# Kernel optimization log

Measured on AMD Instinct MI355X. Metric: run time of the kernel, lower is better.

Reference implementation:

```python
import jax, jax.numpy as jnp
import numpy as np

N_ENT = 50000
N_REL = 500
N_EDGE = 640000
D_IN = 128
D_OUT = 128
NEG_SLOPE = 0.01  # torch nn.LeakyReLU default
BN_EPS = 1e-5


def setup_inputs() -> dict:
    key = jax.random.key(0)
    ks = jax.random.split(key, 16)
    edge_index = jax.random.randint(ks[0], (2, N_EDGE), 0, N_ENT)
    edge_type = jax.random.randint(ks[1], (N_EDGE,), 0, N_REL)
    query_type = jax.random.randint(ks[2], (N_EDGE,), 0, N_REL)
    entity_embed = jax.random.normal(ks[3], (N_ENT, D_IN), jnp.float32)
    rel_embed = jax.random.normal(ks[4], (N_REL, D_IN), jnp.float32)
    s = 0.05
    return {
        "edge_index": edge_index,
        "edge_type": edge_type,
        "query_type": query_type,
        "entity_embed": entity_embed,
        "rel_embed": rel_embed,
        "w_loop": jax.random.normal(ks[5], (D_IN, D_OUT), jnp.float32) * s,
        "w_out": jax.random.normal(ks[6], (D_IN, D_OUT), jnp.float32) * s,
        "w_rel": jax.random.normal(ks[7], (D_IN, D_OUT), jnp.float32) * s,
        "loop_rel": jax.random.normal(ks[8], (1, D_IN), jnp.float32) * s,
        "W_w": jax.random.normal(ks[9], (D_IN, D_IN), jnp.float32) * s,   # W.weight^T layout: x @ W_w
        "W_b": jnp.zeros((D_IN,), jnp.float32),
        "a_w": jax.random.normal(ks[10], (2 * D_IN, 1), jnp.float32) * s,
        "a_b": jnp.zeros((1,), jnp.float32),
        "bias": jnp.zeros((D_OUT,), jnp.float32),
        "bn_gamma": jnp.ones((D_OUT,), jnp.float32),
        "bn_beta": jnp.zeros((D_OUT,), jnp.float32),
    }


def _compgcn_fwd(edge_index, edge_type, query_type, entity_embed, rel_embed,
                 w_loop, w_out, w_rel, loop_rel, W_w, W_b, a_w, a_b,
                 bias, bn_gamma, bn_beta):
    N = entity_embed.shape[0]
    rel_all = jnp.concatenate([rel_embed, loop_rel], axis=0)  # (R+1, D)
    row, col = edge_index[0], edge_index[1]  # values already in [0, N)

    # edge norm: 1/out-degree of source node (deg[row] >= 1 for every edge)
    deg = jax.ops.segment_sum(jnp.ones((row.shape[0],), entity_embed.dtype), row, num_segments=N)
    norm = 1.0 / deg[row]  # (E,)

    # self-loop branch (mode='loop'): rel_transform 'mult' with loop relation, no attention
    loop_res = (entity_embed * rel_all[-1]) @ w_loop  # (N, D_out)

    # out branch (mode='out')
    x_j = entity_embed[col]          # (E, D)
    r_e = rel_all[edge_type]         # (E, D)
    q_e = rel_all[query_type]        # (E, D)
    xj_rel = x_j * r_e               # 'mult' composition

    h = jnp.concatenate([r_e @ W_w + W_b, q_e @ W_w + W_b], axis=-1)  # (E, 2D)
    logits = h @ a_w + a_b                                            # (E, 1)
    alpha = jnp.exp(jax.nn.leaky_relu(logits[:, 0], NEG_SLOPE))       # (E,)
    sum_alpha = jax.ops.segment_sum(alpha, row, num_segments=N)       # (N,)
    alpha = alpha / sum_alpha[row]

    msg = (xj_rel @ w_out) * (alpha * norm)[:, None]                  # (E, D_out)
    out_res = jax.ops.segment_sum(msg, row, num_segments=N)           # (N, D_out)

    out = 0.5 * out_res + 0.5 * loop_res + bias  # dropout = identity (eval)
    # BatchNorm1d, training-mode batch statistics (biased var), over node dim
    mean = jnp.mean(out, axis=0)
    var = jnp.mean((out - mean) ** 2, axis=0)
    out = (out - mean) * jax.lax.rsqrt(var + BN_EPS) * bn_gamma + bn_beta

    ent_out = jax.nn.leaky_relu(out, NEG_SLOPE)
    rel_out = (rel_all @ w_rel)[:-1]
    return ent_out, rel_out


def reference(edge_index, edge_type, query_type, entity_embed, rel_embed,
              w_loop, w_out, w_rel, loop_rel, W_w, W_b, a_w, a_b,
              bias, bn_gamma, bn_beta):
    return _compgcn_fwd(edge_index, edge_type, query_type, entity_embed, rel_embed,
                        w_loop, w_out, w_rel, loop_rel, W_w, W_b, a_w, a_b,
                        bias, bn_gamma, bn_beta)
```

## Files before the change

kernel.cpp:

```cpp
#include <hip/hip_runtime.h>
#include <math.h>

#define E_N 640000
#define N_N 50000
#define R_N 500
#define D   128
#define NEG 0.01f
#define BNEPS 1e-5f
#define CAP 48
#define GROUPS 8
#define RPG 6250

typedef _Float16 f16x8 __attribute__((ext_vector_type(8)));
typedef _Float16 h2 __attribute__((ext_vector_type(2)));
typedef float f32x4 __attribute__((ext_vector_type(4)));

#define CNT_OFF    0u
#define STAT_OFF   50000u
#define ZERO_FLOATS 50256u
#define BUCKET_OFF 50256u
#define ENTH_OFF   4850256u
#define RELH_OFF   8050256u
#define BT_OFF     8082256u
#define S1_OFF     8098640u
#define S2_OFF     8099152u
#define LOOPH_OFF  8099664u

__device__ __forceinline__ float lrelu(float x) { return x > 0.f ? x : NEG * x; }

__device__ __forceinline__ void st_f16x4(_Float16* p, float x, float y, float z, float w) {
    union { _Float16 h[4]; uint2 u; } pk;
    pk.h[0] = (_Float16)x; pk.h[1] = (_Float16)y; pk.h[2] = (_Float16)z; pk.h[3] = (_Float16)w;
    *(uint2*)p = pk.u;
}

__device__ __forceinline__ void st_f16x8(_Float16* p, const float* v) {
    union { _Float16 h[8]; uint4 u; } pk;
#pragma unroll
    for (int j = 0; j < 8; ++j) pk.h[j] = (_Float16)v[j];
    *(uint4*)p = pk.u;
}

#define P1_S   501
#define P1_WB  256
#define P1_REL 500
#define P1_ENT 1563

__global__ __launch_bounds__(128) void k_pre1(const float* __restrict__ Ww,
                                              const float* __restrict__ Wb,
                                              const float* __restrict__ aw,
                                              const float* __restrict__ rel,
                                              const float* __restrict__ looprel,
                                              const float* __restrict__ wout,
                                              const float* __restrict__ wloop,
                                              const float* __restrict__ wrel,
                                              const float* __restrict__ ent,
                                              float* __restrict__ s1,
                                              float* __restrict__ s2,
                                              _Float16* __restrict__ Bt,
                                              float* __restrict__ out_rel,
                                              _Float16* __restrict__ rel_h,
                                              _Float16* __restrict__ ent_h,
                                              _Float16* __restrict__ looprel_h) {
    int b = blockIdx.x, t = threadIdx.x;
    if (b < P1_S) {
        __shared__ float rr[D];
        __shared__ float part[4];
        const float* rp = (b < R_N) ? rel + (size_t)b * D : looprel;
        rr[t] = rp[t];
        if (b < R_N) rel_h[(size_t)b * D + t] = (_Float16)rp[t];
        if (b == R_N) looprel_h[t] = (_Float16)rp[t];
        __syncthreads();
        float v = 0.f;
        for (int i = 0; i < D; ++i) v = fmaf(rr[i], Ww[i * D + t], v);
        float p1 = aw[t] * v + Wb[t] * aw[t];
        float p2 = aw[D + t] * v + Wb[t] * aw[D + t];
        for (int o = 32; o; o >>= 1) {
            p1 += __shfl_down(p1, o);
            p2 += __shfl_down(p2, o);
        }
        if ((t & 63) == 0) {
            part[(t >> 6) * 2] = p1;
            part[(t >> 6) * 2 + 1] = p2;
        }
        __syncthreads();
        if (t == 0) {
            s1[b] = part[0] + part[2];
            s2[b] = part[1] + part[3];
        }
    } else if (b < P1_S + P1_WB) {
        int idx = (b - P1_S) * 128 + t;
        int n = idx & 127, k = idx >> 7;
        float v = (k < D) ? wout[(size_t)k * D + n] : wloop[(size_t)(k - D) * D + n];
        Bt[(size_t)n * 256 + k] = (_Float16)v;
    } else if (b < P1_S + P1_WB + P1_REL) {
        int r = b - (P1_S + P1_WB);
        __shared__ float rr2[D];
        rr2[t] = rel[(size_t)r * D + t];
        __syncthreads();
        float a = 0.f;
        for (int k = 0; k < D; ++k) a = fmaf(rr2[k], wrel[(size_t)k * D + t], a);
        out_rel[(size_t)r * D + t] = a;
    } else {
        int blk = b - (P1_S + P1_WB + P1_REL);
        const float4* e4 = (const float4*)ent;
#pragma unroll
        for (int j = 0; j < 8; ++j) {
            int idx = blk * 1024 + j * 128 + t;
            if (idx < N_N * D / 4) {
                float4 v = e4[idx];
                st_f16x4(ent_h + (size_t)idx * 4, v.x, v.y, v.z, v.w);
            }
        }
    }
}

#define BIN_NCH 313
#define BIN_BLOCKS (BIN_NCH * GROUPS)

__global__ __launch_bounds__(256) void k_bin(const int* __restrict__ row,
                                             const int* __restrict__ col,
                                             const int* __restrict__ et,
                                             const int* __restrict__ qt,
                                             const float* __restrict__ s1,
                                             const float* __restrict__ s2,
                                             const float* __restrict__ ab,
                                             int* __restrict__ cnt,
                                             int2* __restrict__ bucket) {
    int b = blockIdx.x, t = threadIdx.x;
    int g = b & 7;
    int chunk = b >> 3;
    int rlo = g * RPG;
    int e0 = chunk * 2048 + t;
    int r[8];
#pragma unroll
    for (int j = 0; j < 8; ++j) {
        int e = e0 + j * 256;
        r[j] = (e < E_N) ? row[e] : 0x7fffffff;
    }
#pragma unroll
    for (int j = 0; j < 8; ++j) {
        unsigned rr = (unsigned)(r[j] - rlo);
        if (rr < RPG) {
            int e = e0 + j * 256;
            int c = col[e], te = et[e], q = qt[e];
            float a = __expf(lrelu(s1[te] + s2[q] + ab[0]));
            int pos = atomicAdd(&cnt[r[j]], 1);
            if (pos < CAP) {
                bucket[(size_t)r[j] * CAP + pos] =
                    make_int2(c | (te << 16), __float_as_int(a));
            }
        }
    }
}

__global__ __launch_bounds__(128) void k_gather(const int* __restrict__ cnt,
                                                const int2* __restrict__ bucket,
                                                const _Float16* __restrict__ ent_h,
                                                const _Float16* __restrict__ rel_h,
                                                const _Float16* __restrict__ looprel_h,
                                                _Float16* __restrict__ stage) {
    int n = (blockIdx.x & 7) * RPG + (blockIdx.x >> 3);
    int t = threadIdx.x;
    int deg = cnt[n];
    int m = deg < CAP ? deg : CAP;
    __shared__ int eoff[CAP];
    __shared__ int roff[CAP];
    __shared__ h2 sah[CAP];
    __shared__ uint4 xred[16];
    float myv = 0.f;
    if (t < CAP) {
        if (t < m) {
            int2 be = bucket[(size_t)n * CAP + t];
            eoff[t] = (be.x & 0xffff) << 8;
            roff[t] = (be.x >> 16) << 8;
            float a = __int_as_float(be.y);
            myv = a;
            _Float16 ah = (_Float16)a;
            sah[t] = (h2){ah, ah};
        } else {
            eoff[t] = 0; roff[t] = 0;
            sah[t] = (h2){(_Float16)0.f, (_Float16)0.f};
        }
    }
    float suma = myv;
#pragma unroll
    for (int o = 1; o <= 32; o <<= 1) suma += __shfl_xor(suma, o);
    __syncthreads();
    int s = t & 15, g = t >> 4;
    const char* eb = (const char*)ent_h;
    const char* rb = (const char*)rel_h;
    int co = s * 16;
    h2 acc0 = (h2)(_Float16)0.f, acc1 = acc0, acc2 = acc0, acc3 = acc0;
#define EDGE(e_) { \
        uint4 ue = *(const uint4*)(eb + (eoff[e_] + co)); \
        uint4 ur = *(const uint4*)(rb + (roff[e_] + co)); \
        h2 a2 = sah[e_]; \
        const h2* e2 = (const h2*)&ue; \
        const h2* r2 = (const h2*)&ur; \
        acc0 += e2[0] * r2[0] * a2; \
        acc1 += e2[1] * r2[1] * a2; \
        acc2 += e2[2] * r2[2] * a2; \
        acc3 += e2[3] * r2[3] * a2; }
    EDGE(g) EDGE(g + 8)
    if (m > 16) { EDGE(g + 16) EDGE(g + 24) }
    if (m > 32) { EDGE(g + 32) EDGE(g + 40) }
#undef EDGE
#define RED(a_) { \
        unsigned u_ = *(unsigned*)&a_; \
        unsigned v_ = (unsigned)__shfl_xor((int)u_, 16); \
        a_ += *(h2*)&v_; \
        u_ = *(unsigned*)&a_; \
        v_ = (unsigned)__shfl_xor((int)u_, 32); \
        a_ += *(h2*)&v_; }
    RED(acc0) RED(acc1) RED(acc2) RED(acc3)
#undef RED
    if (t >= 64 && t < 80) {
        uint4 u;
        ((h2*)&u)[0] = acc0; ((h2*)&u)[1] = acc1;
        ((h2*)&u)[2] = acc2; ((h2*)&u)[3] = acc3;
        xred[s] = u;
    }
    if (t >= 96 && t < 112) {
        int si = t - 96;
        uint4 ue = *(const uint4*)(eb + ((size_t)n << 8) + si * 16);
        uint4 ul = *(const uint4*)((const char*)looprel_h + si * 16);
        const h2* e2 = (const h2*)&ue;
        const h2* l2 = (const h2*)&ul;
        uint4 o;
#pragma unroll
        for (int w = 0; w < 4; ++w) ((h2*)&o)[w] = e2[w] * l2[w];
        *(uint4*)(stage + (size_t)n * 256 + 128 + si * 8) = o;
    }
    __syncthreads();
    if (t < 16) {
        float inv = (deg > 0) ? 1.0f / (suma * (float)deg) : 0.f;
        uint4 xr = xred[t];
        const h2* x2 = (const h2*)&xr;
        h2 c0 = acc0 + x2[0], c1 = acc1 + x2[1], c2 = acc2 + x2[2], c3 = acc3 + x2[3];
        float v[8] = {(float)c0[0], (float)c0[1], (float)c1[0], (float)c1[1],
                      (float)c2[0], (float)c2[1], (float)c3[0], (float)c3[1]};
#pragma unroll
        for (int j = 0; j < 8; ++j) v[j] *= inv;
        st_f16x8(stage + (size_t)n * 256 + t * 8, v);
    }
}

__global__ __launch_bounds__(256) void k_gemm(const _Float16* stage,
                                              const _Float16* __restrict__ Bt,
                                              const float* __restrict__ bias,
                                              float* out,
                                              float* __restrict__ stat) {
    int t = threadIdx.x;
    int wave = t >> 6, l = t & 63;
    int lm = l & 15, lg = l >> 4;
    size_t mbase = (size_t)blockIdx.x * 128 + wave * 32;
    const f16x8* A = (const f16x8*)stage;
    const f16x8* B = (const f16x8*)Bt;
    f32x4 acc[2][8];
#pragma unroll
    for (int mt = 0; mt < 2; ++mt)
#pragma unroll
        for (int nt = 0; nt < 8; ++nt) acc[mt][nt] = (f32x4)(0.f);
#pragma unroll
    for (int ks = 0; ks < 8; ++ks) {
        f16x8 a0 = A[(mbase + lm) * 32 + ks * 4 + lg];
        f16x8 a1 = A[(mbase + 16 + lm) * 32 + ks * 4 + lg];
#pragma unroll
        for (int nt = 0; nt < 8; ++nt) {
            f16x8 b = B[(size_t)(nt * 16 + lm) * 32 + ks * 4 + lg];
            acc[0][nt] = __builtin_amdgcn_mfma_f32_16x16x32_f16(a0, b, acc[0][nt], 0, 0, 0);
            acc[1][nt] = __builtin_amdgcn_mfma_f32_16x16x32_f16(a1, b, acc[1][nt], 0, 0, 0);
        }
    }
    float psum[8], psq[8];
#pragma unroll
    for (int nt = 0; nt < 8; ++nt) { psum[nt] = 0.f; psq[nt] = 0.f; }
#pragma unroll
    for (int mt = 0; mt < 2; ++mt) {
#pragma unroll
        for (int nt = 0; nt < 8; ++nt) {
            int c = nt * 16 + lm;
            float bv = bias[c];
#pragma unroll
            for (int r = 0; r < 4; ++r) {
                size_t rowi = mbase + mt * 16 + lg * 4 + r;
                if (rowi < N_N) {
                    float v = 0.5f * acc[mt][nt][r] + bv;
                    out[rowi * D + c] = v;
                    psum[nt] += v;
                    psq[nt] += v * v;
                }
            }
        }
    }
    __shared__ float2 red[8][16][16];
    int slot = wave * 4 + lg;
#pragma unroll
    for (int nt = 0; nt < 8; ++nt) red[nt][lm][slot] = make_float2(psum[nt], psq[nt]);
    __syncthreads();
    if (t < 128) {
        int nt = t >> 4, lmm = t & 15;
        float ss = 0.f, qq = 0.f;
#pragma unroll
        for (int k = 0; k < 16; ++k) {
            float2 v = red[nt][lmm][k];
            ss += v.x;
            qq += v.y;
        }
        atomicAdd(&stat[t], ss);
        atomicAdd(&stat[D + t], qq);
    }
}

__global__ __launch_bounds__(256) void k_bnapply(float* __restrict__ out,
                                                 const float* __restrict__ stat,
                                                 const float* __restrict__ gamma,
                                                 const float* __restrict__ beta) {
    __shared__ float ssc[D], ssh[D];
    int t = threadIdx.x;
    if (t < D) {
        float mean = stat[t] * (1.0f / N_N);
        float var = stat[D + t] * (1.0f / N_N) - mean * mean;
        float sc = gamma[t] * rsqrtf(var + BNEPS);
        ssc[t] = sc;
        ssh[t] = beta[t] - mean * sc;
    }
    __syncthreads();
    const float4* sc4 = (const float4*)ssc;
    const float4* sh4 = (const float4*)ssh;
    float4* o4 = (float4*)out;
    const int total = N_N * D / 4;
    for (int i = blockIdx.x * blockDim.x + t; i < total; i += gridDim.x * blockDim.x) {
        int d4 = i & 31;
        float4 v = o4[i];
        float4 s = sc4[d4];
        float4 h = sh4[d4];
        v.x = lrelu(v.x * s.x + h.x);
        v.y = lrelu(v.y * s.y + h.y);
        v.z = lrelu(v.z * s.z + h.z);
        v.w = lrelu(v.w * s.w + h.w);
        o4[i] = v;
    }
}

extern "C" void kernel_launch(void* const* d_in, const int* in_sizes, int n_in,
                              void* d_out, int out_size, void* d_ws, size_t ws_size,
                              hipStream_t stream) {
    const int* edge_index = (const int*)d_in[0];
    const int* row = edge_index;
    const int* col = edge_index + E_N;
    const int* etype = (const int*)d_in[1];
    const int* qtype = (const int*)d_in[2];
    const float* ent = (const float*)d_in[3];
    const float* rel = (const float*)d_in[4];
    const float* w_loop = (const float*)d_in[5];
    const float* w_out = (const float*)d_in[6];
    const float* w_rel = (const float*)d_in[7];
    const float* loop_rel = (const float*)d_in[8];
    const float* W_w = (const float*)d_in[9];
    const float* W_b = (const float*)d_in[10];
    const float* a_w = (const float*)d_in[11];
    const float* a_b = (const float*)d_in[12];
    const float* bias = (const float*)d_in[13];
    const float* bn_gamma = (const float*)d_in[14];
    const float* bn_beta = (const float*)d_in[15];

    float* ws = (float*)d_ws;
    int* cnt = (int*)(ws + CNT_OFF);
    float* stat = ws + STAT_OFF;
    int2* bucket = (int2*)(ws + BUCKET_OFF);
    _Float16* ent_h = (_Float16*)(ws + ENTH_OFF);
    _Float16* rel_h = (_Float16*)(ws + RELH_OFF);
    _Float16* Bt = (_Float16*)(ws + BT_OFF);
    float* s1 = ws + S1_OFF;
    float* s2 = ws + S2_OFF;
    _Float16* looprel_h = (_Float16*)(ws + LOOPH_OFF);

    float* out_ent = (float*)d_out;
    float* out_rel = out_ent + (size_t)N_N * D;
    _Float16* stage = (_Float16*)d_out;

    hipMemsetAsync(d_ws, 0, (size_t)ZERO_FLOATS * sizeof(float), stream);

    k_pre1<<<P1_S + P1_WB + P1_REL + P1_ENT, 128, 0, stream>>>(
        W_w, W_b, a_w, rel, loop_rel, w_out, w_loop, w_rel, ent,
        s1, s2, Bt, out_rel, rel_h, ent_h, looprel_h);
    k_bin<<<BIN_BLOCKS, 256, 0, stream>>>(
        row, col, etype, qtype, s1, s2, a_b, cnt, bucket);
    k_gather<<<N_N, 128, 0, stream>>>(cnt, bucket, ent_h, rel_h, looprel_h, stage);
    k_gemm<<<(N_N + 127) / 128, 256, 0, stream>>>(stage, Bt, bias, out_ent, stat);
    k_bnapply<<<2048, 256, 0, stream>>>(out_ent, stat, bn_gamma, bn_beta);
}
```

Baseline: 136.3 us.

## Fuse edge binning into preprocessing kernel and defer attention exp to gather

Edge binning no longer needs s1/s2, so it is merged into the preprocessing kernel as extra blocks, and one kernel launch with its dependency barrier goes away. Buckets now store the query type instead of the precomputed alpha. The gather kernel reads s1/s2 and computes exp(lrelu(...)) for each edge as it loads the bucket. This lets binning overlap with the weight and embedding conversion work, at the cost of a few extra scattered loads in gather and a smaller per-block binning chunk (128 threads).

```diff
diff --git a/kernel.cpp b/kernel.cpp
--- a/kernel.cpp
+++ b/kernel.cpp
@@ -45,23 +45,32 @@
 #define P1_WB  256
 #define P1_REL 500
 #define P1_ENT 1563
-
-__global__ __launch_bounds__(128) void k_pre1(const float* __restrict__ Ww,
-                                              const float* __restrict__ Wb,
-                                              const float* __restrict__ aw,
-                                              const float* __restrict__ rel,
-                                              const float* __restrict__ looprel,
-                                              const float* __restrict__ wout,
-                                              const float* __restrict__ wloop,
-                                              const float* __restrict__ wrel,
-                                              const float* __restrict__ ent,
-                                              float* __restrict__ s1,
-                                              float* __restrict__ s2,
-                                              _Float16* __restrict__ Bt,
-                                              float* __restrict__ out_rel,
-                                              _Float16* __restrict__ rel_h,
-                                              _Float16* __restrict__ ent_h,
-                                              _Float16* __restrict__ looprel_h) {
+#define P1_TOT (P1_S + P1_WB + P1_REL + P1_ENT)
+#define BIN_BLOCKS (625 * GROUPS)
+#define F1_BLOCKS (P1_TOT + BIN_BLOCKS)
+
+__global__ __launch_bounds__(128) void k_fused1(const float* __restrict__ Ww,
+                                                const float* __restrict__ Wb,
+                                                const float* __restrict__ aw,
+                                                const float* __restrict__ rel,
+                                                const float* __restrict__ looprel,
+                                                const float* __restrict__ wout,
+                                                const float* __restrict__ wloop,
+                                                const float* __restrict__ wrel,
+                                                const float* __restrict__ ent,
+                                                const int* __restrict__ row,
+                                                const int* __restrict__ col,
+                                                const int* __restrict__ et,
+                                                const int* __restrict__ qt,
+                                                float* __restrict__ s1,
+                                                float* __restrict__ s2,
+                                                _Float16* __restrict__ Bt,
+                                                float* __restrict__ out_rel,
+                                                _Float16* __restrict__ rel_h,
+                                                _Float16* __restrict__ ent_h,
+                                                _Float16* __restrict__ looprel_h,
+                                                int* __restrict__ cnt,
+                                                int2* __restrict__ bucket) {
     int b = blockIdx.x, t = threadIdx.x;
     if (b < P1_S) {
         __shared__ float rr[D];
@@ -101,7 +110,7 @@
         float a = 0.f;
         for (int k = 0; k < D; ++k) a = fmaf(rr2[k], wrel[(size_t)k * D + t], a);
         out_rel[(size_t)r * D + t] = a;
-    } else {
+    } else if (b < P1_TOT) {
         int blk = b - (P1_S + P1_WB + P1_REL);
         const float4* e4 = (const float4*)ent;
 #pragma unroll
@@ -112,43 +121,25 @@
                 st_f16x4(ent_h + (size_t)idx * 4, v.x, v.y, v.z, v.w);
             }
         }
-    }
-}
-
-#define BIN_NCH 313
-#define BIN_BLOCKS (BIN_NCH * GROUPS)
-
-__global__ __launch_bounds__(256) void k_bin(const int* __restrict__ row,
-                                             const int* __restrict__ col,
-                                             const int* __restrict__ et,
-                                             const int* __restrict__ qt,
-                                             const float* __restrict__ s1,
-                                             const float* __restrict__ s2,
-                                             const float* __restrict__ ab,
-                                             int* __restrict__ cnt,
-                                             int2* __restrict__ bucket) {
-    int b = blockIdx.x, t = threadIdx.x;
-    int g = b & 7;
-    int chunk = b >> 3;
-    int rlo = g * RPG;
-    int e0 = chunk * 2048 + t;
-    int r[8];
-#pragma unroll
-    for (int j = 0; j < 8; ++j) {
-        int e = e0 + j * 256;
-        r[j] = (e < E_N) ? row[e] : 0x7fffffff;
-    }
-#pragma unroll
-    for (int j = 0; j < 8; ++j) {
-        unsigned rr = (unsigned)(r[j] - rlo);
-        if (rr < RPG) {
-            int e = e0 + j * 256;
-            int c = col[e], te = et[e], q = qt[e];
-            float a = __expf(lrelu(s1[te] + s2[q] + ab[0]));
-            int pos = atomicAdd(&cnt[r[j]], 1);
-            if (pos < CAP) {
-                bucket[(size_t)r[j] * CAP + pos] =
-                    make_int2(c | (te << 16), __float_as_int(a));
+    } else {
+        int gb = b - P1_TOT;
+        int g = gb & 7;
+        int chunk = gb >> 3;
+        int rlo = g * RPG;
+        int e0 = chunk * 1024 + t;
+        int r[8];
+#pragma unroll
+        for (int j = 0; j < 8; ++j) r[j] = row[e0 + j * 128];
+#pragma unroll
+        for (int j = 0; j < 8; ++j) {
+            unsigned rr = (unsigned)(r[j] - rlo);
+            if (rr < RPG) {
+                int e = e0 + j * 128;
+                int c = col[e], te = et[e], q = qt[e];
+                int pos = atomicAdd(&cnt[r[j]], 1);
+                if (pos < CAP) {
+                    bucket[(size_t)r[j] * CAP + pos] = make_int2(c | (te << 16), q);
+                }
             }
         }
     }
@@ -156,6 +147,9 @@
 
 __global__ __launch_bounds__(128) void k_gather(const int* __restrict__ cnt,
                                                 const int2* __restrict__ bucket,
+                                                const float* __restrict__ s1,
+                                                const float* __restrict__ s2,
+                                                const float* __restrict__ ab,
                                                 const _Float16* __restrict__ ent_h,
                                                 const _Float16* __restrict__ rel_h,
                                                 const _Float16* __restrict__ looprel_h,
@@ -172,9 +166,10 @@
     if (t < CAP) {
         if (t < m) {
             int2 be = bucket[(size_t)n * CAP + t];
+            int e_t = be.x >> 16;
             eoff[t] = (be.x & 0xffff) << 8;
-            roff[t] = (be.x >> 16) << 8;
-            float a = __int_as_float(be.y);
+            roff[t] = e_t << 8;
+            float a = __expf(lrelu(s1[e_t] + s2[be.y] + ab[0]));
             myv = a;
             _Float16 ah = (_Float16)a;
             sah[t] = (h2){ah, ah};
@@ -383,12 +378,12 @@
 
     hipMemsetAsync(d_ws, 0, (size_t)ZERO_FLOATS * sizeof(float), stream);
 
-    k_pre1<<<P1_S + P1_WB + P1_REL + P1_ENT, 128, 0, stream>>>(
+    k_fused1<<<F1_BLOCKS, 128, 0, stream>>>(
         W_w, W_b, a_w, rel, loop_rel, w_out, w_loop, w_rel, ent,
-        s1, s2, Bt, out_rel, rel_h, ent_h, looprel_h);
-    k_bin<<<BIN_BLOCKS, 256, 0, stream>>>(
-        row, col, etype, qtype, s1, s2, a_b, cnt, bucket);
-    k_gather<<<N_N, 128, 0, stream>>>(cnt, bucket, ent_h, rel_h, looprel_h, stage);
+        row, col, etype, qtype,
+        s1, s2, Bt, out_rel, rel_h, ent_h, looprel_h, cnt, bucket);
+    k_gather<<<N_N, 128, 0, stream>>>(cnt, bucket, s1, s2, a_b, ent_h, rel_h,
+                                      looprel_h, stage);
     k_gemm<<<(N_N + 127) / 128, 256, 0, stream>>>(stage, Bt, bias, out_ent, stat);
     k_bnapply<<<2048, 256, 0, stream>>>(out_ent, stat, bn_gamma, bn_beta);
 }
```

Result: faster. 132.2 us (-3.0%).
